# Kernel optimization log

Hardware: AMD Instinct MI355X
Metric: run time of the kernel (lower is better)

Reference implementation:

```python
import jax, jax.numpy as jnp
import numpy as np

N = 100000   # num nodes
E = 1200000  # num edges (before self-loops)
K = 2        # SGConv propagation hops


def _gcn_norm(edge_index, edge_weight):
    # PyG gcn_norm: add self-loops (weight 1) then symmetric normalization
    loop = jnp.arange(N, dtype=edge_index.dtype)
    src = jnp.concatenate([edge_index[0], loop])
    dst = jnp.concatenate([edge_index[1], loop])
    w = jnp.concatenate([edge_weight, jnp.ones((N,), edge_weight.dtype)])
    deg = jax.ops.segment_sum(w, dst, num_segments=N)
    dinv = jnp.where(deg > 0, jax.lax.rsqrt(deg), jnp.zeros_like(deg))
    norm = dinv[src] * w * dinv[dst]
    return src, dst, norm


def _sgconv(x, src, dst, norm, W, b):
    # K hops of A_hat @ x, then linear: x @ W.T + b
    for _ in range(K):
        x = jax.ops.segment_sum(norm[:, None] * x[src], dst, num_segments=N)
    return x @ W.T + b


def setup_inputs() -> dict:
    key = jax.random.key(0)
    k = jax.random.split(key, 6)
    d_in, d_hid, d_out = 64, 64, 40
    x = jax.random.normal(k[0], (N, d_in), jnp.float32)
    edge_index = jax.random.randint(k[1], (2, E), 0, N, jnp.int32)
    edge_weight = jnp.ones((E,), jnp.float32)
    W1 = jax.random.normal(k[2], (d_hid, d_in), jnp.float32) / np.sqrt(d_in)
    b1 = jnp.zeros((d_hid,), jnp.float32)
    W2 = jax.random.normal(k[3], (d_out, d_hid), jnp.float32) / np.sqrt(d_hid)
    b2 = jnp.zeros((d_out,), jnp.float32)
    return {"x": x, "edge_index": edge_index, "edge_weight": edge_weight,
            "W1": W1, "b1": b1, "W2": W2, "b2": b2}


def reference(x, edge_index, edge_weight, W1, b1, W2, b2):
    # eval mode: F.dropout(p=0.6, training=False) is identity
    src, dst, norm = _gcn_norm(edge_index, edge_weight)
    h = jax.nn.relu(_sgconv(x, src, dst, norm, W1, b1))
    out = _sgconv(h, src, dst, norm, W2, b2)
    return out
```

## Files before the change

### kernel.cpp

```cpp
#include <hip/hip_runtime.h>
#include <hip/hip_fp16.h>


#define SCAN_TPB 256
#define SCAN_ITEMS 8
#define SCAN_CHUNK (SCAN_TPB * SCAN_ITEMS)
#define P1_EDGES 2048
#define MAX_NB 784


__global__ __launch_bounds__(SCAN_TPB) void scan_partial_kernel(const int* __restrict__ cnt,
                                                                int* __restrict__ bsums, int N_) {
    int t = threadIdx.x;
    int base = blockIdx.x * SCAN_CHUNK + t * SCAN_ITEMS;
    int s = 0;
    #pragma unroll
    for (int j = 0; j < SCAN_ITEMS; ++j) { int i = base + j; if (i < N_) s += cnt[i]; }
    __shared__ int sm[SCAN_TPB];
    sm[t] = s; __syncthreads();
    for (int o = SCAN_TPB / 2; o > 0; o >>= 1) {
        if (t < o) sm[t] += sm[t + o];
        __syncthreads();
    }
    if (t == 0) bsums[blockIdx.x] = sm[0];
}

__global__ __launch_bounds__(1024) void scan_bsums_kernel(int* bsums, int nb,
                                                          int* out, int N_) {
    __shared__ int sm[1024];
    int t = threadIdx.x;
    int v = (t < nb) ? bsums[t] : 0;
    sm[t] = v; __syncthreads();
    for (int o = 1; o < 1024; o <<= 1) {
        int u = (t >= o) ? sm[t - o] : 0;
        __syncthreads();
        sm[t] += u;
        __syncthreads();
    }
    if (t < nb) bsums[t] = sm[t] - v;
    if (t == 1023) out[N_] = sm[1023];
}

__global__ __launch_bounds__(SCAN_TPB) void scan_final_kernel(const int* __restrict__ cnt,
                                                              const int* __restrict__ bsums,
                                                              int* __restrict__ out, int N_) {
    int t = threadIdx.x;
    int base = blockIdx.x * SCAN_CHUNK + t * SCAN_ITEMS;
    int loc[SCAN_ITEMS];
    int s = 0;
    #pragma unroll
    for (int j = 0; j < SCAN_ITEMS; ++j) {
        int i = base + j;
        int c = (i < N_) ? cnt[i] : 0;
        loc[j] = s; s += c;
    }
    __shared__ int sm[SCAN_TPB];
    sm[t] = s; __syncthreads();
    for (int o = 1; o < SCAN_TPB; o <<= 1) {
        int u = (t >= o) ? sm[t - o] : 0;
        __syncthreads();
        sm[t] += u;
        __syncthreads();
    }
    int excl = bsums[blockIdx.x] + sm[t] - s;
    #pragma unroll
    for (int j = 0; j < SCAN_ITEMS; ++j) {
        int i = base + j;
        if (i < N_) out[i] = excl + loc[j];
    }
}

__global__ __launch_bounds__(256) void p1_count_kernel(const int* __restrict__ ei,
                                                       int* __restrict__ coarseCnt,
                                                       int E_, int PB, int NB) {
    __shared__ int hist[MAX_NB];
    int tid = threadIdx.x;
    for (int u = tid; u < NB; u += 256) hist[u] = 0;
    __syncthreads();
    int base = blockIdx.x * P1_EDGES;
    #pragma unroll
    for (int j = 0; j < P1_EDGES / 512; ++j) {
        int e = base + j * 512 + tid * 2;
        if (e + 1 < E_) {
            int2 d2 = *(const int2*)&ei[E_ + e];
            atomicAdd(&hist[d2.x >> 7], 1);
            atomicAdd(&hist[d2.y >> 7], 1);
        } else if (e < E_) {
            atomicAdd(&hist[ei[E_ + e] >> 7], 1);
        }
    }
    __syncthreads();
    for (int u = tid; u < NB; u += 256) coarseCnt[u * PB + blockIdx.x] = hist[u];
}

__global__ __launch_bounds__(256) void p1_scatter_kernel(const int* __restrict__ ei,
                                                         const float* __restrict__ w,
                                                         const int* __restrict__ coarseOff,
                                                         int2* __restrict__ sorted,
                                                         int E_, int PB, int NB) {
    __shared__ int lcur[MAX_NB];
    int tid = threadIdx.x;
    for (int u = tid; u < NB; u += 256) lcur[u] = coarseOff[u * PB + blockIdx.x];
    __syncthreads();
    int base = blockIdx.x * P1_EDGES;
    #pragma unroll
    for (int j = 0; j < P1_EDGES / 512; ++j) {
        int e = base + j * 512 + tid * 2;
        if (e + 1 < E_) {
            int2   s2 = *(const int2*)&ei[e];
            int2   d2 = *(const int2*)&ei[E_ + e];
            float2 w2 = *(const float2*)&w[e];
            int p0 = atomicAdd(&lcur[d2.x >> 7], 1);
            sorted[p0] = make_int2(s2.x | ((d2.x & 127) << 17), __float_as_int(w2.x));
            int p1 = atomicAdd(&lcur[d2.y >> 7], 1);
            sorted[p1] = make_int2(s2.y | ((d2.y & 127) << 17), __float_as_int(w2.y));
        } else if (e < E_) {
            int dst = ei[E_ + e];
            int pos = atomicAdd(&lcur[dst >> 7], 1);
            sorted[pos] = make_int2(ei[e] | ((dst & 127) << 17), __float_as_int(w[e]));
        }
    }
}

__global__ __launch_bounds__(256) void p2_fine_kernel(const int2* __restrict__ sorted,
                                                      const int* __restrict__ coarseOff,
                                                      int2* __restrict__ edge,
                                                      int* __restrict__ row_ptr,
                                                      float* __restrict__ dinv,
                                                      int N_, int E_, int PB, int NB) {
    __shared__ int fcnt[128], fexc[128], fcur[128];
    __shared__ float fdeg[128];
    const int b = blockIdx.x;
    const int tid = threadIdx.x;
    const int start = coarseOff[b * PB];
    const int end = (b + 1 < NB) ? coarseOff[(b + 1) * PB] : E_;
    if (tid < 128) { fcnt[tid] = 0; fdeg[tid] = 1.0f; }
    __syncthreads();
    for (int p = start + tid; p < end; p += 256)
        atomicAdd(&fcnt[sorted[p].x >> 17], 1);
    __syncthreads();
    if (tid < 128) fexc[tid] = fcnt[tid];
    __syncthreads();
    for (int o = 1; o < 128; o <<= 1) {
        int v = (tid < 128 && tid >= o) ? fexc[tid - o] : 0;
        __syncthreads();
        if (tid < 128) fexc[tid] += v;
        __syncthreads();
    }
    const int node0 = b << 7;
    if (tid < 128) {
        fexc[tid] -= fcnt[tid];
        fcur[tid] = 0;
        int node = node0 + tid;
        if (node < N_) row_ptr[node] = start + fexc[tid];
    }
    __syncthreads();
    for (int p = start + tid; p < end; p += 256) {
        int2 pk = sorted[p];
        int fine = pk.x >> 17;
        int src  = pk.x & 0x1FFFF;
        int r = atomicAdd(&fcur[fine], 1);
        atomicAdd(&fdeg[fine], __int_as_float(pk.y));
        edge[start + fexc[fine] + r] = make_int2(src, pk.y);
    }
    __syncthreads();
    if (tid < 128) {
        int node = node0 + tid;
        if (node < N_) {
            float s = fdeg[tid];
            dinv[node] = (s > 0.f) ? (1.0f / sqrtf(s)) : 0.f;
        }
    }
    if (b == 0 && tid == 0) row_ptr[N_] = E_;
}

__global__ __launch_bounds__(256) void scale_csr_kernel(int2* __restrict__ edge,
                                                        const int* __restrict__ row_ptr,
                                                        const float* __restrict__ dinv, int N_) {
    int n = blockIdx.x * blockDim.x + threadIdx.x;
    if (n < N_) {
        float dd = dinv[n];
        int p0 = row_ptr[n], p1 = row_ptr[n + 1];
        for (int p = p0; p < p1; ++p) {
            int2 e = edge[p];
            edge[p].y = __float_as_int(__int_as_float(e.y) * dinv[e.x] * dd);
        }
    }
}

#define FMA_MIX_LO(accv, hbits, vw) \
    asm("v_fma_mix_f32 %0, %1, %2, %0 op_sel_hi:[1,0,0]" : "+v"(accv) : "v"(hbits), "v"(vw))
#define FMA_MIX_HI(accv, hbits, vw) \
    asm("v_fma_mix_f32 %0, %1, %2, %0 op_sel:[1,0,0] op_sel_hi:[1,0,0]" : "+v"(accv) : "v"(hbits), "v"(vw))

template<int NL, int EPI>
__global__ __launch_bounds__(256) void hop_h_kernel(const __half* __restrict__ xin,
                                                    void* __restrict__ xout,
                                                    const float* __restrict__ dinv,
                                                    const int* __restrict__ row_ptr,
                                                    const int2* __restrict__ edge,
                                                    const float* __restrict__ bias, int N_) {
    int wave = (blockIdx.x * blockDim.x + threadIdx.x) >> 6;
    int lane = threadIdx.x & 63;
    const int g   = lane >> 4;
    const int hl  = lane & 15;
    const int hle = (NL == 16) ? hl : min(hl, NL - 1);

    int nd = wave * 4 + g;
    bool real = nd < N_;
    int d = real ? nd : (N_ - 1);

    int e0 = row_ptr[d];
    int nE = real ? (row_ptr[d + 1] - e0) : 0;
    float di = dinv[d];
    float2 selfv = ((const float2*)(xin + (size_t)d * 64))[hle];
    float acc[4] = {0.f, 0.f, 0.f, 0.f};

    int maxNE = nE;
    maxNE = max(maxNE, __shfl_xor(maxNE, 16));
    maxNE = max(maxNE, __shfl_xor(maxNE, 32));

    for (int eb = 0; eb < maxNE; eb += 16) {
        int rem = nE - eb;
        int2 ev = (hl < rem) ? edge[e0 + eb + hl] : make_int2(d, 0);
        int mm = min(16, maxNE - eb);
        for (int j = 0; j < mm; j += 2) {
            int   s0 = __shfl(ev.x, (g << 4) | j);
            int   s1 = __shfl(ev.x, (g << 4) | (j + 1));
            float v0 = __shfl(__int_as_float(ev.y), (g << 4) | j);
            float v1 = __shfl(__int_as_float(ev.y), (g << 4) | (j + 1));
            float2 x0 = ((const float2*)(xin + (size_t)s0 * 64))[hle];
            float2 x1 = ((const float2*)(xin + (size_t)s1 * 64))[hle];
            FMA_MIX_LO(acc[0], x0.x, v0); FMA_MIX_HI(acc[1], x0.x, v0);
            FMA_MIX_LO(acc[2], x0.y, v0); FMA_MIX_HI(acc[3], x0.y, v0);
            FMA_MIX_LO(acc[0], x1.x, v1); FMA_MIX_HI(acc[1], x1.x, v1);
            FMA_MIX_LO(acc[2], x1.y, v1); FMA_MIX_HI(acc[3], x1.y, v1);
        }
    }
    float dii = di * di;
    FMA_MIX_LO(acc[0], selfv.x, dii); FMA_MIX_HI(acc[1], selfv.x, dii);
    FMA_MIX_LO(acc[2], selfv.y, dii); FMA_MIX_HI(acc[3], selfv.y, dii);

    if (real && hl < NL) {
        if constexpr (EPI == 0) {
            float2 pk;
            ((__half2*)&pk)[0] = __floats2half2_rn(acc[0], acc[1]);
            ((__half2*)&pk)[1] = __floats2half2_rn(acc[2], acc[3]);
            ((float2*)((__half*)xout + (size_t)d * 64))[hl] = pk;
        } else if constexpr (EPI == 1) {
            float4 bv = ((const float4*)bias)[hl];
            float2 pk;
            ((__half2*)&pk)[0] = __floats2half2_rn(fmaxf(acc[0] + bv.x, 0.f),
                                                   fmaxf(acc[1] + bv.y, 0.f));
            ((__half2*)&pk)[1] = __floats2half2_rn(fmaxf(acc[2] + bv.z, 0.f),
                                                   fmaxf(acc[3] + bv.w, 0.f));
            ((float2*)((__half*)xout + (size_t)d * 64))[hl] = pk;
        } else {
            float4 bv = ((const float4*)bias)[hl];
            float4 r = make_float4(acc[0] + bv.x, acc[1] + bv.y,
                                   acc[2] + bv.z, acc[3] + bv.w);
            *(float4*)((float*)xout + (size_t)d * 40 + hl * 4) = r;
        }
    }
}

template<int F, bool INH>
__global__ __launch_bounds__(256, 4) void linear_tiled_kernel(const void* __restrict__ hin,
                                                              __half* __restrict__ outp,
                                                              const float* __restrict__ W,
                                                              int N_) {
    constexpr int BM = 64;
    __shared__ float hs[BM * 64];
    __shared__ float ws[64 * 64];
    const int tid  = threadIdx.x;
    const int base = blockIdx.x * BM;

    for (int u = tid; u < 64 * 16; u += 256) {
        int f = u >> 4, kc = u & 15;
        float4 v = (f < F) ? ((const float4*)W)[f * 16 + kc]
                           : make_float4(0.f, 0.f, 0.f, 0.f);
        *(float4*)&ws[f * 64 + ((kc ^ ((f >> 2) & 7)) << 2)] = v;
    }
    const int lim = min(BM, N_ - base);
    for (int u = tid; u < BM * 16; u += 256) {
        int n = u >> 4, kc = u & 15;
        float4 v;
        if (n < lim) {
            if constexpr (INH) {
                float2 hv = ((const float2*)((const __half*)hin + (size_t)(base + n) * 64))[kc];
                const __half2* hh = (const __half2*)&hv;
                float2 a = __half22float2(hh[0]);
                float2 b = __half22float2(hh[1]);
                v = make_float4(a.x, a.y, b.x, b.y);
            } else {
                v = ((const float4*)((const float*)hin + (size_t)(base + n) * 64))[kc];
            }
        } else v = make_float4(0.f, 0.f, 0.f, 0.f);
        *(float4*)&hs[n * 64 + ((kc ^ ((n >> 2) & 7)) << 2)] = v;
    }
    __syncthreads();

    const int f0 = (tid & 15) << 2;
    const int n0 = (tid >> 4) << 2;
    float4 acc[4];
    #pragma unroll
    for (int i = 0; i < 4; ++i) acc[i] = make_float4(0.f, 0.f, 0.f, 0.f);

    #pragma unroll 2
    for (int kc = 0; kc < 16; ++kc) {
        float4 hv[4], wv[4];
        #pragma unroll
        for (int i = 0; i < 4; ++i) {
            int n = n0 + i;
            hv[i] = *(const float4*)&hs[n * 64 + ((kc ^ ((n >> 2) & 7)) << 2)];
        }
        #pragma unroll
        for (int j = 0; j < 4; ++j) {
            int f = f0 + j;
            wv[j] = *(const float4*)&ws[f * 64 + ((kc ^ ((f >> 2) & 7)) << 2)];
        }
        #pragma unroll
        for (int i = 0; i < 4; ++i) {
            acc[i].x = fmaf(hv[i].x, wv[0].x, acc[i].x);
            acc[i].x = fmaf(hv[i].y, wv[0].y, acc[i].x);
            acc[i].x = fmaf(hv[i].z, wv[0].z, acc[i].x);
            acc[i].x = fmaf(hv[i].w, wv[0].w, acc[i].x);
            acc[i].y = fmaf(hv[i].x, wv[1].x, acc[i].y);
            acc[i].y = fmaf(hv[i].y, wv[1].y, acc[i].y);
            acc[i].y = fmaf(hv[i].z, wv[1].z, acc[i].y);
            acc[i].y = fmaf(hv[i].w, wv[1].w, acc[i].y);
            acc[i].z = fmaf(hv[i].x, wv[2].x, acc[i].z);
            acc[i].z = fmaf(hv[i].y, wv[2].y, acc[i].z);
            acc[i].z = fmaf(hv[i].z, wv[2].z, acc[i].z);
            acc[i].z = fmaf(hv[i].w, wv[2].w, acc[i].z);
            acc[i].w = fmaf(hv[i].x, wv[3].x, acc[i].w);
            acc[i].w = fmaf(hv[i].y, wv[3].y, acc[i].w);
            acc[i].w = fmaf(hv[i].z, wv[3].z, acc[i].w);
            acc[i].w = fmaf(hv[i].w, wv[3].w, acc[i].w);
        }
    }

    if (f0 < F) {
        #pragma unroll
        for (int i = 0; i < 4; ++i) {
            int n = base + n0 + i;
            if (n < N_) {
                __half* o = outp + (size_t)n * 64 + f0;
                ((__half2*)o)[0] = __floats2half2_rn(acc[i].x, acc[i].y);
                ((__half2*)o)[1] = __floats2half2_rn(acc[i].z, acc[i].w);
            }
        }
    }
}

extern "C" void kernel_launch(void* const* d_in, const int* in_sizes, int n_in,
                              void* d_out, int out_size, void* d_ws, size_t ws_size,
                              hipStream_t stream) {
    const float* x   = (const float*)d_in[0];
    const int*   ei  = (const int*)d_in[1];
    const float* w   = (const float*)d_in[2];
    const float* W1  = (const float*)d_in[3];
    const float* b1  = (const float*)d_in[4];
    const float* W2  = (const float*)d_in[5];
    const float* b2  = (const float*)d_in[6];
    float* out = (float*)d_out;

    const int N_ = in_sizes[0] / 64;
    const int E_ = in_sizes[2];
    const int PB = (E_ + P1_EDGES - 1) / P1_EDGES;
    const int NB = (N_ + 127) >> 7;
    const int M  = NB * PB;

    char* ws = (char*)d_ws;
    size_t off = 0;
    auto alloc = [&](size_t bytes) { size_t o = off; off += (bytes + 255) & ~(size_t)255; return o; };
    float* dinv      = (float*)(ws + alloc((size_t)N_ * 4));
    int*   row_ptr   = (int*)  (ws + alloc(((size_t)N_ + 1) * 4));
    int*   bsums     = (int*)  (ws + alloc(1024 * 4));
    int*   coarseCnt = (int*)  (ws + alloc((size_t)M * 4));
    int*   coarseOff = (int*)  (ws + alloc(((size_t)M + 1) * 4));
    int2*  edge      = (int2*) (ws + alloc((size_t)E_ * 8));
    float* bufA      = (float*)(ws + alloc((size_t)N_ * 64 * 4));
    float* bufB      = (float*)(ws + alloc((size_t)N_ * 64 * 4));
    int2*   sorted = (int2*)bufA;
    __half* hA0    = (__half*)bufA;
    __half* hLo    = (__half*)bufB;
    __half* hHi    = (__half*)((char*)bufB + (size_t)N_ * 64 * 2);
    (void)ws_size; (void)n_in; (void)out_size;

    const int bn = (N_ + 255) / 256;
    const int bh4 = (N_ + 15) / 16;
    const int nbs = (M + SCAN_CHUNK - 1) / SCAN_CHUNK;
    const int bl_ = (N_ + 63) / 64;

    p1_count_kernel<<<PB, 256, 0, stream>>>(ei, coarseCnt, E_, PB, NB);
    scan_partial_kernel<<<nbs, SCAN_TPB, 0, stream>>>(coarseCnt, bsums, M);
    scan_bsums_kernel<<<1, 1024, 0, stream>>>(bsums, nbs, coarseOff, M);
    scan_final_kernel<<<nbs, SCAN_TPB, 0, stream>>>(coarseCnt, bsums, coarseOff, M);
    p1_scatter_kernel<<<PB, 256, 0, stream>>>(ei, w, coarseOff, sorted, E_, PB, NB);
    p2_fine_kernel<<<NB, 256, 0, stream>>>(sorted, coarseOff, edge, row_ptr, dinv, N_, E_, PB, NB);
    scale_csr_kernel<<<bn, 256, 0, stream>>>(edge, row_ptr, dinv, N_);

    linear_tiled_kernel<64, false><<<bl_, 256, 0, stream>>>(x, hLo, W1, N_);
    hop_h_kernel<16, 0><<<bh4, 256, 0, stream>>>(hLo, hHi, dinv, row_ptr, edge, nullptr, N_);
    hop_h_kernel<16, 1><<<bh4, 256, 0, stream>>>(hHi, hA0, dinv, row_ptr, edge, b1, N_);
    linear_tiled_kernel<40, true><<<bl_, 256, 0, stream>>>(hA0, hLo, W2, N_);
    hop_h_kernel<10, 0><<<bh4, 256, 0, stream>>>(hLo, hHi, dinv, row_ptr, edge, nullptr, N_);
    hop_h_kernel<10, 2><<<bh4, 256, 0, stream>>>(hHi, out, dinv, row_ptr, edge, b2, N_);
}
```

Before: 221.9 us.

## Factor symmetric normalization into node scaling and drop CSR scaling kernel

```diff
diff --git a/kernel.cpp b/kernel.cpp
--- a/kernel.cpp
+++ b/kernel.cpp
@@ -172,20 +172,6 @@
         }
     }
     if (b == 0 && tid == 0) row_ptr[N_] = E_;
-}
-
-__global__ __launch_bounds__(256) void scale_csr_kernel(int2* __restrict__ edge,
-                                                        const int* __restrict__ row_ptr,
-                                                        const float* __restrict__ dinv, int N_) {
-    int n = blockIdx.x * blockDim.x + threadIdx.x;
-    if (n < N_) {
-        float dd = dinv[n];
-        int p0 = row_ptr[n], p1 = row_ptr[n + 1];
-        for (int p = p0; p < p1; ++p) {
-            int2 e = edge[p];
-            edge[p].y = __float_as_int(__int_as_float(e.y) * dinv[e.x] * dd);
-        }
-    }
 }
 
 #define FMA_MIX_LO(accv, hbits, vw) \
@@ -237,9 +223,13 @@
             FMA_MIX_LO(acc[2], x1.y, v1); FMA_MIX_HI(acc[3], x1.y, v1);
         }
     }
-    float dii = di * di;
-    FMA_MIX_LO(acc[0], selfv.x, dii); FMA_MIX_HI(acc[1], selfv.x, dii);
-    FMA_MIX_LO(acc[2], selfv.y, dii); FMA_MIX_HI(acc[3], selfv.y, dii);
+    const float one = 1.0f;
+    FMA_MIX_LO(acc[0], selfv.x, one); FMA_MIX_HI(acc[1], selfv.x, one);
+    FMA_MIX_LO(acc[2], selfv.y, one); FMA_MIX_HI(acc[3], selfv.y, one);
+
+    float sc = (EPI == 0) ? di * di : di;
+    #pragma unroll
+    for (int u = 0; u < 4; ++u) acc[u] *= sc;
 
     if (real && hl < NL) {
         if constexpr (EPI == 0) {
@@ -268,6 +258,7 @@
 __global__ __launch_bounds__(256, 4) void linear_tiled_kernel(const void* __restrict__ hin,
                                                               __half* __restrict__ outp,
                                                               const float* __restrict__ W,
+                                                              const float* __restrict__ dinv,
                                                               int N_) {
     constexpr int BM = 64;
     __shared__ float hs[BM * 64];
@@ -345,9 +336,10 @@
         for (int i = 0; i < 4; ++i) {
             int n = base + n0 + i;
             if (n < N_) {
+                float dn = dinv[n];
                 __half* o = outp + (size_t)n * 64 + f0;
-                ((__half2*)o)[0] = __floats2half2_rn(acc[i].x, acc[i].y);
-                ((__half2*)o)[1] = __floats2half2_rn(acc[i].z, acc[i].w);
+                ((__half2*)o)[0] = __floats2half2_rn(acc[i].x * dn, acc[i].y * dn);
+                ((__half2*)o)[1] = __floats2half2_rn(acc[i].z * dn, acc[i].w * dn);
             }
         }
     }
@@ -388,7 +380,6 @@
     __half* hHi    = (__half*)((char*)bufB + (size_t)N_ * 64 * 2);
     (void)ws_size; (void)n_in; (void)out_size;
 
-    const int bn = (N_ + 255) / 256;
     const int bh4 = (N_ + 15) / 16;
     const int nbs = (M + SCAN_CHUNK - 1) / SCAN_CHUNK;
     const int bl_ = (N_ + 63) / 64;
@@ -399,12 +390,11 @@
     scan_final_kernel<<<nbs, SCAN_TPB, 0, stream>>>(coarseCnt, bsums, coarseOff, M);
     p1_scatter_kernel<<<PB, 256, 0, stream>>>(ei, w, coarseOff, sorted, E_, PB, NB);
     p2_fine_kernel<<<NB, 256, 0, stream>>>(sorted, coarseOff, edge, row_ptr, dinv, N_, E_, PB, NB);
-    scale_csr_kernel<<<bn, 256, 0, stream>>>(edge, row_ptr, dinv, N_);
-
-    linear_tiled_kernel<64, false><<<bl_, 256, 0, stream>>>(x, hLo, W1, N_);
+
+    linear_tiled_kernel<64, false><<<bl_, 256, 0, stream>>>(x, hLo, W1, dinv, N_);
     hop_h_kernel<16, 0><<<bh4, 256, 0, stream>>>(hLo, hHi, dinv, row_ptr, edge, nullptr, N_);
     hop_h_kernel<16, 1><<<bh4, 256, 0, stream>>>(hHi, hA0, dinv, row_ptr, edge, b1, N_);
-    linear_tiled_kernel<40, true><<<bl_, 256, 0, stream>>>(hA0, hLo, W2, N_);
+    linear_tiled_kernel<40, true><<<bl_, 256, 0, stream>>>(hA0, hLo, W2, dinv, N_);
     hop_h_kernel<10, 0><<<bh4, 256, 0, stream>>>(hLo, hHi, dinv, row_ptr, edge, nullptr, N_);
     hop_h_kernel<10, 2><<<bh4, 256, 0, stream>>>(hHi, out, dinv, row_ptr, edge, b2, N_);
 }
```

Result: faster. 207.9 us (-6.3%).
